# Kernel tuning notes

Hardware: AMD Instinct MI355X
Metric: run time of the kernel (lower is better)

The kernel has to match this reference:

```python
import jax, jax.numpy as jnp
import numpy as np


def setup_inputs() -> dict:
    key = jax.random.key(0)
    kZ, kQ, kW, kU, kbk = jax.random.split(key, 5)
    B, E, D = 64, 16, 64
    N_ATOMS = 200000
    N_NP = 160000
    N_BK = 20000
    Q_DIM = 64
    Z = jax.random.normal(kZ, (B, E, D), dtype=jnp.float32)
    Q = jax.random.normal(kQ, (B, Q_DIM), dtype=jnp.float32)
    W = jax.random.normal(kW, (N_NP, D), dtype=jnp.float32)
    U = jax.random.normal(kU, (N_NP, Q_DIM), dtype=jnp.float32)
    np_indices = jnp.arange(N_NP, dtype=jnp.int64 if jax.config.jax_enable_x64 else jnp.int32)
    bk_indices = jax.random.randint(kbk, (N_BK,), 0, N_ATOMS, dtype=jnp.int32)
    return {"Z": Z, "Q": Q, "W": W, "U": U,
            "np_indices": np_indices, "bk_indices": bk_indices,
            "n_atoms": N_ATOMS}


def reference(Z, Q, W, U, np_indices, bk_indices, n_atoms):
    # Batched valuation for all neural-predicate atoms at once:
    # vm(Z, Q, atom_i) = sigmoid(sum_{e,d} Z[b,e,d] * W[i,d] + Q[b] . U[i])
    scores = jax.nn.sigmoid(jnp.einsum('bed,nd->bn', Z, W) + Q @ U.T)  # [B, n_np]
    B = Z.shape[0]
    V = jnp.zeros((B, n_atoms), dtype=jnp.float32)
    V = V.at[:, 0].set(1.0)                 # V[:, 0] = 1.0 (true atom)
    V = V.at[:, np_indices].set(scores)     # scatter valuation outputs
    V = V.at[:, bk_indices].add(1.0)        # background knowledge atoms += 1
    return V
```

## Files before the change

### kernel.cpp

```cpp
#include <hip/hip_runtime.h>


typedef _Float16 half8_t __attribute__((ext_vector_type(8)));
typedef _Float16 half4_t __attribute__((ext_vector_type(4)));
typedef float float4_t __attribute__((ext_vector_type(4)));

#define E_DIM 16
#define D_DIM 64
#define QD    64

__global__ void prep_kernel(const float* __restrict__ Z, const float* __restrict__ Q,
                            const int* __restrict__ bk, int n_bk,
                            _Float16* __restrict__ Afrag, float* __restrict__ cnt) {
    int blk = blockIdx.x;
    int tid = threadIdx.x;
    if (blk < 32) {
        int t = blk * 256 + tid;
        int b = t >> 7, k = t & 127;
        float v;
        if (k < D_DIM) {
            const float* zp = Z + (size_t)b * E_DIM * D_DIM + k;
            v = 0.f;
            #pragma unroll
            for (int e = 0; e < E_DIM; ++e) v += zp[e * D_DIM];
        } else {
            v = Q[b * QD + (k - D_DIM)];
        }
        int mt = b >> 4, r = b & 15;
        int kq = k >> 5, j = k & 7, quad = (k >> 3) & 3;
        int lane = r + quad * 16;
        Afrag[(((mt * 4 + kq) * 64) + lane) * 8 + j] = (_Float16)v;
    } else if (cnt) {
        int i = (blk - 32) * 256 + tid;
        if (i < n_bk) atomicAdd(&cnt[bk[i]], 1.0f);
    }
}

#define WH_STRIDE 72
#define ET_STRIDE 68

__global__ __launch_bounds__(256) void main_kernel(
        const float* __restrict__ W, const float* __restrict__ U,
        const _Float16* __restrict__ Afrag, const float* __restrict__ cnt,
        float* __restrict__ V, int n_np, int n_atoms) {
    __shared__ __align__(16) char smem_raw[2 * 64 * WH_STRIDE * 2];
    int tid = threadIdx.x;
    long long nblk = (long long)blockIdx.x * 64;
    int c  = tid & 15;
    int rr = tid >> 4;

    if (nblk >= n_np) {
        float4_t cn4 = {0.f, 0.f, 0.f, 0.f};
        if (cnt) cn4 = *(const float4_t*)(cnt + nblk + 4 * c);
        #pragma unroll
        for (int p = 0; p < 4; ++p) {
            int row = p * 16 + rr;
            *(float4_t*)(V + (size_t)row * n_atoms + nblk + 4 * c) = cn4;
        }
        return;
    }

    _Float16(*Wh)[WH_STRIDE] = (_Float16(*)[WH_STRIDE])smem_raw;
    _Float16(*Uh)[WH_STRIDE] = (_Float16(*)[WH_STRIDE])(smem_raw + 64 * WH_STRIDE * 2);

    int wv = tid >> 6, lane = tid & 63;
    int quad = lane >> 4, l15 = lane & 15;

    const half8_t* Ap = (const half8_t*)Afrag;
    half8_t a[4][4];
    #pragma unroll
    for (int mt = 0; mt < 4; ++mt)
        #pragma unroll
        for (int kq = 0; kq < 4; ++kq)
            a[mt][kq] = Ap[(mt * 4 + kq) * 64 + lane];

    const float4_t* Wg = (const float4_t*)(W + (size_t)nblk * D_DIM);
    const float4_t* Ug = (const float4_t*)(U + (size_t)nblk * QD);
    #pragma unroll
    for (int i = 0; i < 4; ++i) {
        int j = tid + i * 256;
        int row = j >> 4, k = (j & 15) * 4;
        float4_t w = Wg[j], u = Ug[j];
        half4_t wh, uh;
        #pragma unroll
        for (int q = 0; q < 4; ++q) { wh[q] = (_Float16)w[q]; uh[q] = (_Float16)u[q]; }
        *(half4_t*)&Wh[row][k] = wh;
        *(half4_t*)&Uh[row][k] = uh;
    }
    __syncthreads();

    int rB = wv * 16 + l15;
    half8_t b0 = *(const half8_t*)&Wh[rB][quad * 8];
    half8_t b1 = *(const half8_t*)&Wh[rB][32 + quad * 8];
    half8_t b2 = *(const half8_t*)&Uh[rB][quad * 8];
    half8_t b3 = *(const half8_t*)&Uh[rB][32 + quad * 8];

    float4_t acc[4] = {{0.f,0.f,0.f,0.f},{0.f,0.f,0.f,0.f},
                       {0.f,0.f,0.f,0.f},{0.f,0.f,0.f,0.f}};
    #pragma unroll
    for (int mt = 0; mt < 4; ++mt) {
        acc[mt] = __builtin_amdgcn_mfma_f32_16x16x32_f16(a[mt][0], b0, acc[mt], 0, 0, 0);
        acc[mt] = __builtin_amdgcn_mfma_f32_16x16x32_f16(a[mt][1], b1, acc[mt], 0, 0, 0);
        acc[mt] = __builtin_amdgcn_mfma_f32_16x16x32_f16(a[mt][2], b2, acc[mt], 0, 0, 0);
        acc[mt] = __builtin_amdgcn_mfma_f32_16x16x32_f16(a[mt][3], b3, acc[mt], 0, 0, 0);
    }

    __syncthreads();
    float(*eT)[ET_STRIDE] = (float(*)[ET_STRIDE])smem_raw;

    #pragma unroll
    for (int mt = 0; mt < 4; ++mt)
        #pragma unroll
        for (int r = 0; r < 4; ++r)
            eT[mt * 16 + quad * 4 + r][wv * 16 + l15] = acc[mt][r];
    __syncthreads();

    float4_t cn4 = {0.f, 0.f, 0.f, 0.f};
    if (cnt) cn4 = *(const float4_t*)(cnt + nblk + 4 * c);
    #pragma unroll
    for (int p = 0; p < 4; ++p) {
        int row = p * 16 + rr;
        float4_t v = *(const float4_t*)&eT[row][4 * c];
        float4_t s;
        #pragma unroll
        for (int q = 0; q < 4; ++q)
            s[q] = 1.0f / (1.0f + __expf(-v[q])) + cn4[q];
        *(float4_t*)(V + (size_t)row * n_atoms + nblk + 4 * c) = s;
    }
}

__global__ void bk_scatter(const int* __restrict__ bk, int n_bk,
                           float* __restrict__ V, int n_atoms) {
    int i = blockIdx.x * 256 + threadIdx.x;
    if (i < n_bk)
        atomicAdd(&V[(size_t)blockIdx.y * n_atoms + bk[i]], 1.0f);
}

extern "C" void kernel_launch(void* const* d_in, const int* in_sizes, int n_in,
                              void* d_out, int out_size, void* d_ws, size_t ws_size,
                              hipStream_t stream) {
    const float* Z = (const float*)d_in[0];
    const float* Q = (const float*)d_in[1];
    const float* W = (const float*)d_in[2];
    const float* U = (const float*)d_in[3];
    const int* bk = (const int*)d_in[5];
    float* V = (float*)d_out;

    int B       = in_sizes[0] / (E_DIM * D_DIM);
    int n_np    = in_sizes[2] / D_DIM;
    int n_bk    = in_sizes[5];
    int n_atoms = out_size / B;

    _Float16* Afrag = (_Float16*)d_ws;
    size_t need = 16384 + (size_t)n_atoms * sizeof(float);
    bool use_cnt = ws_size >= need;
    float* cnt = use_cnt ? (float*)((char*)d_ws + 16384) : nullptr;

    if (use_cnt) {
        hipMemsetAsync(cnt, 0, (size_t)n_atoms * sizeof(float), stream);
        int cnt_blocks = (n_bk + 255) / 256;
        prep_kernel<<<32 + cnt_blocks, 256, 0, stream>>>(Z, Q, bk, n_bk, Afrag, cnt);
    } else {
        prep_kernel<<<32, 256, 0, stream>>>(Z, Q, bk, n_bk, Afrag, nullptr);
    }

    int nb = n_atoms / 64;
    main_kernel<<<nb, 256, 0, stream>>>(W, U, Afrag, cnt, V, n_np, n_atoms);

    if (!use_cnt) {
        dim3 g((n_bk + 255) / 256, B);
        bk_scatter<<<g, 256, 0, stream>>>(bk, n_bk, V, n_atoms);
    }
}
```

Measured before the change: 138.8 us.

## Process two 64-atom tiles per block with double-buffered W/U loads and nontemporal stores

Each GEMM block now handles 128 atoms as two 64-row stages. The second stage's W/U global loads are issued before the first stage's MFMAs and written to a second shared-memory buffer, so load latency overlaps compute. Output writes to V use nontemporal stores to avoid polluting cache with the large streaming output. This halves the number of GEMM blocks and doubles shared memory per block, which may reduce occupancy, and it assumes n_np is a multiple of 128.

```diff
diff --git a/kernel.cpp b/kernel.cpp
--- a/kernel.cpp
+++ b/kernel.cpp
@@ -38,34 +38,73 @@
 
 #define WH_STRIDE 72
 #define ET_STRIDE 68
+#define BUF_BYTES (2 * 64 * WH_STRIDE * 2)
+
+__device__ __forceinline__ void stage_load(const float* __restrict__ W,
+                                           const float* __restrict__ U,
+                                           long long sb, int tid,
+                                           float4_t* wr, float4_t* ur) {
+    const float4_t* Wg = (const float4_t*)(W + sb * D_DIM);
+    const float4_t* Ug = (const float4_t*)(U + sb * QD);
+    #pragma unroll
+    for (int i = 0; i < 4; ++i) {
+        wr[i] = Wg[tid + i * 256];
+        ur[i] = Ug[tid + i * 256];
+    }
+}
+
+__device__ __forceinline__ void stage_write(char* buf, int tid,
+                                            const float4_t* wr, const float4_t* ur) {
+    _Float16(*Wh)[WH_STRIDE] = (_Float16(*)[WH_STRIDE])buf;
+    _Float16(*Uh)[WH_STRIDE] = (_Float16(*)[WH_STRIDE])(buf + 64 * WH_STRIDE * 2);
+    #pragma unroll
+    for (int i = 0; i < 4; ++i) {
+        int j = tid + i * 256;
+        int row = j >> 4, k = (j & 15) * 4;
+        half4_t wh, uh;
+        #pragma unroll
+        for (int q = 0; q < 4; ++q) {
+            wh[q] = (_Float16)wr[i][q];
+            uh[q] = (_Float16)ur[i][q];
+        }
+        *(half4_t*)&Wh[row][k] = wh;
+        *(half4_t*)&Uh[row][k] = uh;
+    }
+}
 
 __global__ __launch_bounds__(256) void main_kernel(
         const float* __restrict__ W, const float* __restrict__ U,
         const _Float16* __restrict__ Afrag, const float* __restrict__ cnt,
-        float* __restrict__ V, int n_np, int n_atoms) {
-    __shared__ __align__(16) char smem_raw[2 * 64 * WH_STRIDE * 2];
+        float* __restrict__ V, int n_np, int n_atoms, int n_gemm_blocks) {
+    __shared__ __align__(16) char smem_raw[2 * BUF_BYTES];
     int tid = threadIdx.x;
-    long long nblk = (long long)blockIdx.x * 64;
+    int bid = blockIdx.x;
     int c  = tid & 15;
     int rr = tid >> 4;
 
-    if (nblk >= n_np) {
+    if (bid >= n_gemm_blocks) {
+        long long nblk = (long long)n_np + (long long)(bid - n_gemm_blocks) * 64;
         float4_t cn4 = {0.f, 0.f, 0.f, 0.f};
         if (cnt) cn4 = *(const float4_t*)(cnt + nblk + 4 * c);
         #pragma unroll
         for (int p = 0; p < 4; ++p) {
             int row = p * 16 + rr;
-            *(float4_t*)(V + (size_t)row * n_atoms + nblk + 4 * c) = cn4;
+            __builtin_nontemporal_store(cn4,
+                (float4_t*)(V + (size_t)row * n_atoms + nblk + 4 * c));
         }
         return;
     }
 
-    _Float16(*Wh)[WH_STRIDE] = (_Float16(*)[WH_STRIDE])smem_raw;
-    _Float16(*Uh)[WH_STRIDE] = (_Float16(*)[WH_STRIDE])(smem_raw + 64 * WH_STRIDE * 2);
-
+    long long base = (long long)bid * 128;
     int wv = tid >> 6, lane = tid & 63;
     int quad = lane >> 4, l15 = lane & 15;
 
+    float4_t cn4[2] = {{0.f,0.f,0.f,0.f},{0.f,0.f,0.f,0.f}};
+    if (cnt) {
+        cn4[0] = *(const float4_t*)(cnt + base + 4 * c);
+        cn4[1] = *(const float4_t*)(cnt + base + 64 + 4 * c);
+    }
+
     const half8_t* Ap = (const half8_t*)Afrag;
     half8_t a[4][4];
     #pragma unroll
@@ -74,58 +113,60 @@
         for (int kq = 0; kq < 4; ++kq)
             a[mt][kq] = Ap[(mt * 4 + kq) * 64 + lane];
 
-    const float4_t* Wg = (const float4_t*)(W + (size_t)nblk * D_DIM);
-    const float4_t* Ug = (const float4_t*)(U + (size_t)nblk * QD);
-    #pragma unroll
-    for (int i = 0; i < 4; ++i) {
-        int j = tid + i * 256;
-        int row = j >> 4, k = (j & 15) * 4;
-        float4_t w = Wg[j], u = Ug[j];
-        half4_t wh, uh;
-        #pragma unroll
-        for (int q = 0; q < 4; ++q) { wh[q] = (_Float16)w[q]; uh[q] = (_Float16)u[q]; }
-        *(half4_t*)&Wh[row][k] = wh;
-        *(half4_t*)&Uh[row][k] = uh;
-    }
+    float4_t w0[4], u0[4], w1[4], u1[4];
+    stage_load(W, U, base, tid, w0, u0);
+    stage_write(smem_raw, tid, w0, u0);
     __syncthreads();
 
     int rB = wv * 16 + l15;
-    half8_t b0 = *(const half8_t*)&Wh[rB][quad * 8];
-    half8_t b1 = *(const half8_t*)&Wh[rB][32 + quad * 8];
-    half8_t b2 = *(const half8_t*)&Uh[rB][quad * 8];
-    half8_t b3 = *(const half8_t*)&Uh[rB][32 + quad * 8];
-
-    float4_t acc[4] = {{0.f,0.f,0.f,0.f},{0.f,0.f,0.f,0.f},
-                       {0.f,0.f,0.f,0.f},{0.f,0.f,0.f,0.f}};
-    #pragma unroll
-    for (int mt = 0; mt < 4; ++mt) {
-        acc[mt] = __builtin_amdgcn_mfma_f32_16x16x32_f16(a[mt][0], b0, acc[mt], 0, 0, 0);
-        acc[mt] = __builtin_amdgcn_mfma_f32_16x16x32_f16(a[mt][1], b1, acc[mt], 0, 0, 0);
-        acc[mt] = __builtin_amdgcn_mfma_f32_16x16x32_f16(a[mt][2], b2, acc[mt], 0, 0, 0);
-        acc[mt] = __builtin_amdgcn_mfma_f32_16x16x32_f16(a[mt][3], b3, acc[mt], 0, 0, 0);
-    }
-
-    __syncthreads();
-    float(*eT)[ET_STRIDE] = (float(*)[ET_STRIDE])smem_raw;
-
-    #pragma unroll
-    for (int mt = 0; mt < 4; ++mt)
-        #pragma unroll
-        for (int r = 0; r < 4; ++r)
-            eT[mt * 16 + quad * 4 + r][wv * 16 + l15] = acc[mt][r];
-    __syncthreads();
-
-    float4_t cn4 = {0.f, 0.f, 0.f, 0.f};
-    if (cnt) cn4 = *(const float4_t*)(cnt + nblk + 4 * c);
-    #pragma unroll
-    for (int p = 0; p < 4; ++p) {
-        int row = p * 16 + rr;
-        float4_t v = *(const float4_t*)&eT[row][4 * c];
-        float4_t s;
-        #pragma unroll
-        for (int q = 0; q < 4; ++q)
-            s[q] = 1.0f / (1.0f + __expf(-v[q])) + cn4[q];
-        *(float4_t*)(V + (size_t)row * n_atoms + nblk + 4 * c) = s;
+    #pragma unroll
+    for (int s = 0; s < 2; ++s) {
+        char* cbuf = smem_raw + s * BUF_BYTES;
+        _Float16(*Wh)[WH_STRIDE] = (_Float16(*)[WH_STRIDE])cbuf;
+        _Float16(*Uh)[WH_STRIDE] = (_Float16(*)[WH_STRIDE])(cbuf + 64 * WH_STRIDE * 2);
+
+        if (s == 0) stage_load(W, U, base + 64, tid, w1, u1);
+
+        half8_t b0 = *(const half8_t*)&Wh[rB][quad * 8];
+        half8_t b1 = *(const half8_t*)&Wh[rB][32 + quad * 8];
+        half8_t b2 = *(const half8_t*)&Uh[rB][quad * 8];
+        half8_t b3 = *(const half8_t*)&Uh[rB][32 + quad * 8];
+
+        float4_t acc[4] = {{0.f,0.f,0.f,0.f},{0.f,0.f,0.f,0.f},
+                           {0.f,0.f,0.f,0.f},{0.f,0.f,0.f,0.f}};
+        #pragma unroll
+        for (int mt = 0; mt < 4; ++mt) {
+            acc[mt] = __builtin_amdgcn_mfma_f32_16x16x32_f16(a[mt][0], b0, acc[mt], 0, 0, 0);
+            acc[mt] = __builtin_amdgcn_mfma_f32_16x16x32_f16(a[mt][1], b1, acc[mt], 0, 0, 0);
+            acc[mt] = __builtin_amdgcn_mfma_f32_16x16x32_f16(a[mt][2], b2, acc[mt], 0, 0, 0);
+            acc[mt] = __builtin_amdgcn_mfma_f32_16x16x32_f16(a[mt][3], b3, acc[mt], 0, 0, 0);
+        }
+
+        if (s == 0) stage_write(smem_raw + BUF_BYTES, tid, w1, u1);
+
+        __syncthreads();
+
+        float(*eT)[ET_STRIDE] = (float(*)[ET_STRIDE])cbuf;
+
+        #pragma unroll
+        for (int mt = 0; mt < 4; ++mt)
+            #pragma unroll
+            for (int r = 0; r < 4; ++r)
+                eT[mt * 16 + quad * 4 + r][wv * 16 + l15] = acc[mt][r];
+        __syncthreads();
+
+        long long nblk = base + s * 64;
+        #pragma unroll
+        for (int p = 0; p < 4; ++p) {
+            int row = p * 16 + rr;
+            float4_t v = *(const float4_t*)&eT[row][4 * c];
+            float4_t out;
+            #pragma unroll
+            for (int q = 0; q < 4; ++q)
+                out[q] = 1.0f / (1.0f + __expf(-v[q])) + cn4[s][q];
+            __builtin_nontemporal_store(out,
+                (float4_t*)(V + (size_t)row * n_atoms + nblk + 4 * c));
+        }
     }
 }
 
@@ -164,8 +205,10 @@
         prep_kernel<<<32, 256, 0, stream>>>(Z, Q, bk, n_bk, Afrag, nullptr);
     }
 
-    int nb = n_atoms / 64;
-    main_kernel<<<nb, 256, 0, stream>>>(W, U, Afrag, cnt, V, n_np, n_atoms);
+    int gb = n_np / 128;
+    int tail_blocks = (n_atoms - n_np) / 64;
+    main_kernel<<<gb + tail_blocks, 256, 0, stream>>>(W, U, Afrag, cnt, V,
+                                                      n_np, n_atoms, gb);
 
     if (!use_cnt) {
         dim3 g((n_bk + 255) / 256, B);
```

Result: no change. 138.4 us (-0.3%).

## Process four strips per block with register-prefetched W/U and double-buffered LDS

Applied to the files above, without the earlier changes.

Each GEMM block now handles four 64-atom strips instead of one. It loads W and U directly from global memory into registers in MFMA fragment layout, prefetching the next strip while the current one computes, so the shared-memory staging and its sync are no longer needed. The A fragments are loaded once per block and reused across strips, and a double-buffered transpose buffer leaves one barrier per strip. The cost is fewer blocks (less parallelism), more registers per thread, and a reliance on n_np being divisible by 256.

```diff
diff --git a/kernel.cpp b/kernel.cpp
--- a/kernel.cpp
+++ b/kernel.cpp
@@ -2,12 +2,13 @@
 
 
 typedef _Float16 half8_t __attribute__((ext_vector_type(8)));
-typedef _Float16 half4_t __attribute__((ext_vector_type(4)));
 typedef float float4_t __attribute__((ext_vector_type(4)));
 
 #define E_DIM 16
 #define D_DIM 64
 #define QD    64
+#define NS    4
+#define ET_STRIDE 68
 
 __global__ void prep_kernel(const float* __restrict__ Z, const float* __restrict__ Q,
                             const int* __restrict__ bk, int n_bk,
@@ -36,20 +37,18 @@
     }
 }
 
-#define WH_STRIDE 72
-#define ET_STRIDE 68
-
 __global__ __launch_bounds__(256) void main_kernel(
         const float* __restrict__ W, const float* __restrict__ U,
         const _Float16* __restrict__ Afrag, const float* __restrict__ cnt,
-        float* __restrict__ V, int n_np, int n_atoms) {
-    __shared__ __align__(16) char smem_raw[2 * 64 * WH_STRIDE * 2];
+        float* __restrict__ V, int n_np, int n_atoms, int n_gemm_blocks) {
+    __shared__ __align__(16) float eT[2][64][ET_STRIDE];
     int tid = threadIdx.x;
-    long long nblk = (long long)blockIdx.x * 64;
+    int bid = blockIdx.x;
     int c  = tid & 15;
     int rr = tid >> 4;
 
-    if (nblk >= n_np) {
+    if (bid >= n_gemm_blocks) {
+        long long nblk = (long long)n_np + (long long)(bid - n_gemm_blocks) * 64;
         float4_t cn4 = {0.f, 0.f, 0.f, 0.f};
         if (cnt) cn4 = *(const float4_t*)(cnt + nblk + 4 * c);
         #pragma unroll
@@ -60,11 +59,10 @@
         return;
     }
 
-    _Float16(*Wh)[WH_STRIDE] = (_Float16(*)[WH_STRIDE])smem_raw;
-    _Float16(*Uh)[WH_STRIDE] = (_Float16(*)[WH_STRIDE])(smem_raw + 64 * WH_STRIDE * 2);
-
+    long long base = (long long)bid * (64 * NS);
     int wv = tid >> 6, lane = tid & 63;
     int quad = lane >> 4, l15 = lane & 15;
+    int rB = wv * 16 + l15;
 
     const half8_t* Ap = (const half8_t*)Afrag;
     half8_t a[4][4];
@@ -74,58 +72,68 @@
         for (int kq = 0; kq < 4; ++kq)
             a[mt][kq] = Ap[(mt * 4 + kq) * 64 + lane];
 
-    const float4_t* Wg = (const float4_t*)(W + (size_t)nblk * D_DIM);
-    const float4_t* Ug = (const float4_t*)(U + (size_t)nblk * QD);
-    #pragma unroll
-    for (int i = 0; i < 4; ++i) {
-        int j = tid + i * 256;
-        int row = j >> 4, k = (j & 15) * 4;
-        float4_t w = Wg[j], u = Ug[j];
-        half4_t wh, uh;
-        #pragma unroll
-        for (int q = 0; q < 4; ++q) { wh[q] = (_Float16)w[q]; uh[q] = (_Float16)u[q]; }
-        *(half4_t*)&Wh[row][k] = wh;
-        *(half4_t*)&Uh[row][k] = uh;
-    }
-    __syncthreads();
+    const float4_t* Wg = (const float4_t*)W;
+    const float4_t* Ug = (const float4_t*)U;
 
-    int rB = wv * 16 + l15;
-    half8_t b0 = *(const half8_t*)&Wh[rB][quad * 8];
-    half8_t b1 = *(const half8_t*)&Wh[rB][32 + quad * 8];
-    half8_t b2 = *(const half8_t*)&Uh[rB][quad * 8];
-    half8_t b3 = *(const half8_t*)&Uh[rB][32 + quad * 8];
+    float4_t wb[2][4], ub[2][4];
+    auto load_strip = [&](int s, float4_t wr[4], float4_t ur[4]) {
+        size_t o = ((size_t)(base + s * 64 + rB)) * 16 + quad * 2;
+        wr[0] = Wg[o];     wr[1] = Wg[o + 1];
+        wr[2] = Wg[o + 8]; wr[3] = Wg[o + 9];
+        ur[0] = Ug[o];     ur[1] = Ug[o + 1];
+        ur[2] = Ug[o + 8]; ur[3] = Ug[o + 9];
+    };
 
-    float4_t acc[4] = {{0.f,0.f,0.f,0.f},{0.f,0.f,0.f,0.f},
-                       {0.f,0.f,0.f,0.f},{0.f,0.f,0.f,0.f}};
-    #pragma unroll
-    for (int mt = 0; mt < 4; ++mt) {
-        acc[mt] = __builtin_amdgcn_mfma_f32_16x16x32_f16(a[mt][0], b0, acc[mt], 0, 0, 0);
-        acc[mt] = __builtin_amdgcn_mfma_f32_16x16x32_f16(a[mt][1], b1, acc[mt], 0, 0, 0);
-        acc[mt] = __builtin_amdgcn_mfma_f32_16x16x32_f16(a[mt][2], b2, acc[mt], 0, 0, 0);
-        acc[mt] = __builtin_amdgcn_mfma_f32_16x16x32_f16(a[mt][3], b3, acc[mt], 0, 0, 0);
-    }
-
-    __syncthreads();
-    float(*eT)[ET_STRIDE] = (float(*)[ET_STRIDE])smem_raw;
+    load_strip(0, wb[0], ub[0]);
 
     #pragma unroll
-    for (int mt = 0; mt < 4; ++mt)
+    for (int s = 0; s < NS; ++s) {
+        if (s + 1 < NS) load_strip(s + 1, wb[(s + 1) & 1], ub[(s + 1) & 1]);
+
+        float4_t cn4 = {0.f, 0.f, 0.f, 0.f};
+        if (cnt) cn4 = *(const float4_t*)(cnt + base + s * 64 + 4 * c);
+
+        half8_t b0, b1, b2, b3;
         #pragma unroll
-        for (int r = 0; r < 4; ++r)
-            eT[mt * 16 + quad * 4 + r][wv * 16 + l15] = acc[mt][r];
-    __syncthreads();
+        for (int q = 0; q < 4; ++q) {
+            b0[q]     = (_Float16)wb[s & 1][0][q];
+            b0[q + 4] = (_Float16)wb[s & 1][1][q];
+            b1[q]     = (_Float16)wb[s & 1][2][q];
+            b1[q + 4] = (_Float16)wb[s & 1][3][q];
+            b2[q]     = (_Float16)ub[s & 1][0][q];
+            b2[q + 4] = (_Float16)ub[s & 1][1][q];
+            b3[q]     = (_Float16)ub[s & 1][2][q];
+            b3[q + 4] = (_Float16)ub[s & 1][3][q];
+        }
 
-    float4_t cn4 = {0.f, 0.f, 0.f, 0.f};
-    if (cnt) cn4 = *(const float4_t*)(cnt + nblk + 4 * c);
-    #pragma unroll
-    for (int p = 0; p < 4; ++p) {
-        int row = p * 16 + rr;
-        float4_t v = *(const float4_t*)&eT[row][4 * c];
-        float4_t s;
+        float4_t acc[4] = {{0.f,0.f,0.f,0.f},{0.f,0.f,0.f,0.f},
+                           {0.f,0.f,0.f,0.f},{0.f,0.f,0.f,0.f}};
         #pragma unroll
-        for (int q = 0; q < 4; ++q)
-            s[q] = 1.0f / (1.0f + __expf(-v[q])) + cn4[q];
-        *(float4_t*)(V + (size_t)row * n_atoms + nblk + 4 * c) = s;
+        for (int mt = 0; mt < 4; ++mt) {
+            acc[mt] = __builtin_amdgcn_mfma_f32_16x16x32_f16(a[mt][0], b0, acc[mt], 0, 0, 0);
+            acc[mt] = __builtin_amdgcn_mfma_f32_16x16x32_f16(a[mt][1], b1, acc[mt], 0, 0, 0);
+            acc[mt] = __builtin_amdgcn_mfma_f32_16x16x32_f16(a[mt][2], b2, acc[mt], 0, 0, 0);
+            acc[mt] = __builtin_amdgcn_mfma_f32_16x16x32_f16(a[mt][3], b3, acc[mt], 0, 0, 0);
+        }
+
+        #pragma unroll
+        for (int mt = 0; mt < 4; ++mt)
+            #pragma unroll
+            for (int r = 0; r < 4; ++r)
+                eT[s & 1][mt * 16 + quad * 4 + r][wv * 16 + l15] = acc[mt][r];
+        __syncthreads();
+
+        long long nblk = base + s * 64;
+        #pragma unroll
+        for (int p = 0; p < 4; ++p) {
+            int row = p * 16 + rr;
+            float4_t v = *(const float4_t*)&eT[s & 1][row][4 * c];
+            float4_t out;
+            #pragma unroll
+            for (int q = 0; q < 4; ++q)
+                out[q] = 1.0f / (1.0f + __expf(-v[q])) + cn4[q];
+            *(float4_t*)(V + (size_t)row * n_atoms + nblk + 4 * c) = out;
+        }
     }
 }
 
@@ -164,8 +172,10 @@
         prep_kernel<<<32, 256, 0, stream>>>(Z, Q, bk, n_bk, Afrag, nullptr);
     }
 
-    int nb = n_atoms / 64;
-    main_kernel<<<nb, 256, 0, stream>>>(W, U, Afrag, cnt, V, n_np, n_atoms);
+    int gb = n_np / (64 * NS);
+    int tail_blocks = (n_atoms - n_np) / 64;
+    main_kernel<<<gb + tail_blocks, 256, 0, stream>>>(W, U, Afrag, cnt, V,
+                                                      n_np, n_atoms, gb);
 
     if (!use_cnt) {
         dim3 g((n_bk + 255) / 256, B);
```

New measurement: 140.5 us. Within noise of the previous version (+1.3%).
